# Optimization experiments

Measured on AMD Instinct MI355X. Metric: run time of the kernel, lower is better.

Reference implementation:

```python
import jax, jax.numpy as jnp
import numpy as np

DIM = 768
HEADS = 12
HIDDEN = 3072  # dim * mlp_ratio
EPS = 1e-5


def layernorm(x, g, b):
    mu = jnp.mean(x, axis=-1, keepdims=True)
    var = jnp.var(x, axis=-1, keepdims=True)
    return (x - mu) * jax.lax.rsqrt(var + EPS) * g + b


def setup_inputs() -> dict:
    key = jax.random.key(0)
    ks = jax.random.split(key, 10)
    s = 0.02
    return {
        "x": jax.random.normal(ks[0], (4, 1024, DIM), jnp.float32),
        "attention_mask": jax.random.randint(ks[1], (4, 1024), 0, 2, jnp.int32),
        "ln1_g": jnp.ones((DIM,), jnp.float32),
        "ln1_b": jnp.zeros((DIM,), jnp.float32),
        "ln2_g": jnp.ones((DIM,), jnp.float32),
        "ln2_b": jnp.zeros((DIM,), jnp.float32),
        "w_qkv": jax.random.normal(ks[2], (DIM, 3 * DIM), jnp.float32) * s,
        "b_qkv": jnp.zeros((3 * DIM,), jnp.float32),
        "w_proj": jax.random.normal(ks[3], (DIM, DIM), jnp.float32) * s,
        "b_proj": jnp.zeros((DIM,), jnp.float32),
        "w_fc1": jax.random.normal(ks[4], (DIM, HIDDEN), jnp.float32) * s,
        "b_fc1": jnp.zeros((HIDDEN,), jnp.float32),
        "w_fc2": jax.random.normal(ks[5], (HIDDEN, DIM), jnp.float32) * s,
        "b_fc2": jnp.zeros((DIM,), jnp.float32),
    }


def reference(x, attention_mask, ln1_g, ln1_b, ln2_g, ln2_b,
              w_qkv, b_qkv, w_proj, b_proj, w_fc1, b_fc1, w_fc2, b_fc2):
    B, N, C = x.shape
    hd = C // HEADS
    scale = hd ** -0.5

    # --- attention branch ---
    h = layernorm(x, ln1_g, ln1_b)
    qkv = (h @ w_qkv + b_qkv).reshape(B, N, 3, HEADS, hd)
    q, k, v = qkv[:, :, 0], qkv[:, :, 1], qkv[:, :, 2]  # [B,N,H,hd]
    attn = jnp.einsum('bnhd,bmhd->bhnm', q, k) * scale
    mask_bias = jnp.where(attention_mask == 0, -10000.0, 0.0)[:, None, None, :]
    attn = jax.nn.softmax(attn + mask_bias, axis=-1)
    o = jnp.einsum('bhnm,bmhd->bnhd', attn, v).reshape(B, N, C)
    x = x + (o @ w_proj + b_proj)

    # --- MLP branch ---
    h = layernorm(x, ln2_g, ln2_b)
    h = jax.nn.gelu(h @ w_fc1 + b_fc1, approximate=False)
    x = x + (h @ w_fc2 + b_fc2)
    return x
```

## Files before the change

### kernel.cpp

```cpp
#include <hip/hip_runtime.h>

#define DIM 768
#define NTOK 4096
#define HID 3072

typedef __attribute__((ext_vector_type(8))) short bf16x8;
typedef __attribute__((ext_vector_type(4))) float f32x4;

__device__ inline unsigned short f2bf(float f){
  unsigned u = __float_as_uint(f);
  u += 0x7fff + ((u >> 16) & 1);
  return (unsigned short)(u >> 16);
}
__device__ inline unsigned cvt_pk_bf16(float a, float b){
  unsigned r;
  asm("v_cvt_pk_bf16_f32 %0, %1, %2" : "=v"(r) : "v"(a), "v"(b));
  return r;
}
__device__ inline void gload_lds16(const void* g, void* l){
  __builtin_amdgcn_global_load_lds(
      (const __attribute__((address_space(1))) unsigned int*)g,
      (__attribute__((address_space(3))) unsigned int*)l, 16, 0, 0);
}
template<int N> __device__ inline void wait_vmcnt(){
  if constexpr (N == 0) asm volatile("s_waitcnt vmcnt(0)" ::: "memory");
  else if constexpr (N == 4) asm volatile("s_waitcnt vmcnt(4)" ::: "memory");
  else if constexpr (N == 8) asm volatile("s_waitcnt vmcnt(8)" ::: "memory");
  else static_assert(N == 0, "unsupported vmcnt");
}
__device__ inline int swz_read(int row, int hi){
  return (row * 64 + hi * 16) ^ ((row & 7) << 4);
}

__global__ __launch_bounds__(256) void ln_kernel(const float* __restrict__ x,
    const float* __restrict__ g, const float* __restrict__ b,
    unsigned short* __restrict__ out)
{
  int row = blockIdx.x * 4 + (threadIdx.x >> 6);
  int lane = threadIdx.x & 63;
  const float* xr = x + (size_t)row * DIM;
  float4 v[3];
  float s = 0.f, s2 = 0.f;
#pragma unroll
  for (int j = 0; j < 3; ++j){
    v[j] = *(const float4*)(xr + j * 256 + lane * 4);
    s  += v[j].x + v[j].y + v[j].z + v[j].w;
    s2 += v[j].x*v[j].x + v[j].y*v[j].y + v[j].z*v[j].z + v[j].w*v[j].w;
  }
#pragma unroll
  for (int m = 1; m < 64; m <<= 1){ s += __shfl_xor(s, m, 64); s2 += __shfl_xor(s2, m, 64); }
  float mu  = s * (1.f / 768.f);
  float var = s2 * (1.f / 768.f) - mu * mu;
  float inv = rsqrtf(var + 1e-5f);
#pragma unroll
  for (int j = 0; j < 3; ++j){
    int c0 = j * 256 + lane * 4;
    float vv[4] = { v[j].x, v[j].y, v[j].z, v[j].w };
    ushort4 o4;
    o4.x = f2bf((vv[0] - mu) * inv * g[c0 + 0] + b[c0 + 0]);
    o4.y = f2bf((vv[1] - mu) * inv * g[c0 + 1] + b[c0 + 1]);
    o4.z = f2bf((vv[2] - mu) * inv * g[c0 + 2] + b[c0 + 2]);
    o4.w = f2bf((vv[3] - mu) * inv * g[c0 + 3] + b[c0 + 3]);
    *(ushort4*)(out + (size_t)row * DIM + c0) = o4;
  }
}

__global__ __launch_bounds__(256) void transpose4_kernel(
    const float* __restrict__ w_qkv, const float* __restrict__ w_proj,
    const float* __restrict__ w_fc1, const float* __restrict__ w_fc2,
    unsigned short* __restrict__ tq, unsigned short* __restrict__ tp,
    unsigned short* __restrict__ t1, unsigned short* __restrict__ t2)
{
  __shared__ __align__(16) unsigned short tile[32][33];
  int id = blockIdx.x;
  const float* W; unsigned short* Wt; int K, N, tx_n;
  if (id < 1728)      { W = w_qkv;  Wt = tq; K = 768;  N = 2304; tx_n = 72; }
  else if (id < 2304) { W = w_proj; Wt = tp; K = 768;  N = 768;  tx_n = 24; id -= 1728; }
  else if (id < 4608) { W = w_fc1;  Wt = t1; K = 768;  N = 3072; tx_n = 96; id -= 2304; }
  else                { W = w_fc2;  Wt = t2; K = 3072; N = 768;  tx_n = 24; id -= 4608; }
  int n0 = (id % tx_n) * 32, k0 = (id / tx_n) * 32;
  int tx = threadIdx.x & 31, ty = threadIdx.x >> 5;
#pragma unroll
  for (int i = 0; i < 32; i += 8)
    tile[ty + i][tx] = f2bf(W[(size_t)(k0 + ty + i) * N + n0 + tx]);
  __syncthreads();
#pragma unroll
  for (int i = 0; i < 32; i += 8)
    Wt[(size_t)(n0 + ty + i) * K + k0 + tx] = tile[tx][ty + i];
}

__global__ __launch_bounds__(256) void pack_mask_kernel(const int* __restrict__ am,
    unsigned long long* __restrict__ pm)
{
  int lane = threadIdx.x & 63, w = threadIdx.x >> 6, b = blockIdx.x;
  for (int k = w; k < 16; k += 4){
    unsigned long long m = __ballot(am[b * 1024 + k * 64 + lane] != 0);
    if (lane == 0) pm[b * 16 + k] = m;
  }
}

template<int DEPTH, int EPI, typename OutT>
__global__ __launch_bounds__(256) void gemm_kernel(
    const unsigned short* __restrict__ A,
    const unsigned short* __restrict__ Bt,
    const float* __restrict__ bias,
    OutT* __restrict__ C,
    unsigned short* __restrict__ q_out,
    unsigned short* __restrict__ k_out,
    unsigned short* __restrict__ v_out,
    int M, int N, int K)
{
  constexpr int BM = 128, BN = 128, BK = 32, WM = 64, WN = 64;
  constexpr int WAVES_N = BN / WN;
  constexpr int MI = WM / 16, NI = WN / 16;
  constexpr int ACH = BM * BK / 8, BCH = BN * BK / 8;
  constexpr int NC = (ACH + BCH) / 256;
  constexpr int SMEM_B = DEPTH * (BM + BN) * BK * 2;
  __shared__ __align__(16) char smem[SMEM_B];
  auto As = (unsigned short(*)[BM * BK])smem;
  auto Bs = (unsigned short(*)[BN * BK])(smem + DEPTH * BM * BK * 2);
  const int t = threadIdx.x, lane = t & 63, wid = t >> 6;
  const int lo = lane & 15, hi = lane >> 4;
  const int wr = wid / WAVES_N, wc = wid % WAVES_N;

  const int gx = gridDim.x;
  const int nwg = gx * gridDim.y;
  const int lin = blockIdx.y * gx + blockIdx.x;
  const int swz = (lin & 7) * (nwg >> 3) + (lin >> 3);
  const int bm = (swz / gx) * BM, bn = (swz % gx) * BN;

  auto stage = [&](int buf, int k0){
#pragma unroll
    for (int u = 0; u < NC; ++u){
      int c = u * 256 + t;
      if (c < ACH){
        int rp = c >> 2, r = rp ^ ((rp >> 2) & 1), q = (c & 3) ^ (r & 3);
        gload_lds16(A + (size_t)(bm + r) * K + k0 + q * 8, &As[buf][c * 8]);
      } else {
        int c2 = c - ACH;
        int rp = c2 >> 2, r = rp ^ ((rp >> 2) & 1), q = (c2 & 3) ^ (r & 3);
        gload_lds16(Bt + (size_t)(bn + r) * K + k0 + q * 8, &Bs[buf][c2 * 8]);
      }
    }
  };

  f32x4 acc[MI][NI];
#pragma unroll
  for (int i = 0; i < MI; ++i)
#pragma unroll
    for (int j = 0; j < NI; ++j) acc[i][j] = (f32x4){0.f, 0.f, 0.f, 0.f};

  const int NIT = K / BK;
#pragma unroll
  for (int d = 0; d < DEPTH - 1; ++d) stage(d, d * BK);
  for (int it = 0; it < NIT; ++it){
    int rem = NIT - 1 - it;
    if (rem >= DEPTH - 2) wait_vmcnt<(DEPTH - 2) * NC>();
    else wait_vmcnt<0>();
    __builtin_amdgcn_sched_barrier(0);
    __builtin_amdgcn_s_barrier();
    __builtin_amdgcn_sched_barrier(0);
    if (it + DEPTH - 1 < NIT) stage((it + DEPTH - 1) % DEPTH, (it + DEPTH - 1) * BK);
    const char* as = (const char*)As[it % DEPTH];
    const char* bs = (const char*)Bs[it % DEPTH];
    bf16x8 af[MI], bfr[NI];
#pragma unroll
    for (int i = 0; i < MI; ++i){
      int row = wr * WM + i * 16 + lo;
      af[i] = *(const bf16x8*)(as + swz_read(row, hi));
    }
#pragma unroll
    for (int j = 0; j < NI; ++j){
      int row = wc * WN + j * 16 + lo;
      bfr[j] = *(const bf16x8*)(bs + swz_read(row, hi));
    }
#pragma unroll
    for (int i = 0; i < MI; ++i)
#pragma unroll
      for (int j = 0; j < NI; ++j)
        acc[i][j] = __builtin_amdgcn_mfma_f32_16x16x32_bf16(af[i], bfr[j], acc[i][j], 0, 0, 0);
  }

  __syncthreads();

  if constexpr (EPI == 0 || EPI == 1){
    constexpr int LDE = BN + 8;
    unsigned short* ET = (unsigned short*)smem;
#pragma unroll
    for (int i = 0; i < MI; ++i)
#pragma unroll
      for (int j = 0; j < NI; ++j){
        float bcol = bias[bn + wc * WN + j * 16 + lo];
#pragma unroll
        for (int r = 0; r < 4; ++r){
          float v = acc[i][j][r] + bcol;
          if constexpr (EPI == 1) v = 0.5f * v * (1.f + erff(v * 0.70710678118f));
          ET[(wr * WM + i * 16 + hi * 4 + r) * LDE + wc * WN + j * 16 + lo] = f2bf(v);
        }
      }
    __syncthreads();
#pragma unroll
    for (int p = 0; p < BM / 16; ++p){
      int row = p * 16 + (t >> 4), chunk = t & 15;
      *(bf16x8*)&((unsigned short*)C)[(size_t)(bm + row) * N + bn + chunk * 8] =
          *(const bf16x8*)&ET[row * LDE + chunk * 8];
    }
  } else {
    constexpr int LDE = BN + 8;
    unsigned short* ET = (unsigned short*)smem;
    const int part = bn / 768;
    const int cloc = bn % 768;
#pragma unroll
    for (int i = 0; i < MI; ++i)
#pragma unroll
      for (int j = 0; j < NI; ++j){
        int col_l = wc * WN + j * 16 + lo;
        float bcol = bias[bn + col_l];
#pragma unroll
        for (int r = 0; r < 4; ++r){
          int row_l = wr * WM + i * 16 + hi * 4 + r;
          unsigned short us = f2bf(acc[i][j][r] + bcol);
          if (part < 2) ET[row_l * LDE + col_l] = us;
          else          ET[col_l * LDE + row_l] = us;
        }
      }
    __syncthreads();
    const int bb = bm >> 10, n0b = bm & 1023;
    if (part < 2){
      unsigned short* dst0 = (part == 0) ? q_out : k_out;
#pragma unroll
      for (int p = 0; p < 8; ++p){
        int row = p * 16 + (t >> 4), chunk = t & 15;
        int hh = cloc / 64 + (chunk >> 3), d0 = (chunk & 7) * 8;
        unsigned short* dst = dst0 + ((size_t)(bb * 12 + hh)) * 65536 + (n0b + row) * 64 + d0;
        *(bf16x8*)dst = *(const bf16x8*)&ET[row * LDE + chunk * 8];
      }
    } else {
#pragma unroll
      for (int p = 0; p < 8; ++p){
        int colg = p * 16 + (t >> 4), chunk = t & 15;
        int hh = cloc / 64 + (colg >> 6), d = colg & 63;
        unsigned short* dst = v_out + ((size_t)(bb * 12 + hh)) * 65536 + (size_t)d * 1024 + n0b + chunk * 8;
        *(bf16x8*)dst = *(const bf16x8*)&ET[colg * LDE + chunk * 8];
      }
    }
  }
}

__global__ __launch_bounds__(512) void gemm_ks_kernel(
    const unsigned short* __restrict__ A,
    const unsigned short* __restrict__ Bt,
    const float* __restrict__ bias,
    const float* __restrict__ resid,
    float* __restrict__ C,
    int M, int N, int K)
{
  constexpr int BM = 128, BN = 96, BK = 64, DEPTH = 3;
  constexpr int MI = 4, NI = 3;
  constexpr int ACH = BM * BK / 8;
  constexpr int BCH = BN * BK / 8;
  constexpr int NC = 4;
  constexpr int TILE_A = BM * BK * 2, TILE_B = BN * BK * 2;
  constexpr int LDE = BN + 4;
  constexpr int SMEM_B = (DEPTH * (TILE_A + TILE_B) > BM * LDE * 4)
                       ?  DEPTH * (TILE_A + TILE_B) : BM * LDE * 4;
  __shared__ __align__(16) char smem[SMEM_B];
  auto As = (unsigned short(*)[BM * BK])smem;
  auto Bs = (unsigned short(*)[BN * BK])(smem + DEPTH * TILE_A);
  const int t = threadIdx.x, lane = t & 63, wid = t >> 6;
  const int lo = lane & 15, hi = lane >> 4;
  const int ks = wid & 1, wc = (wid >> 1) & 1, wr = wid >> 2;

  const int gx = gridDim.x;
  const int nwg = gx * gridDim.y;
  const int lin = blockIdx.y * gx + blockIdx.x;
  const int swz = (lin & 7) * (nwg >> 3) + (lin >> 3);
  const int bm = (swz / gx) * BM, bn = (swz % gx) * BN;

  auto stage = [&](int buf, int k0){
#pragma unroll
    for (int u = 0; u < NC; ++u){
      int c = u * 512 + t;
      if (c < ACH){
        int r = c >> 3, q = (c & 7) ^ (r & 7);
        gload_lds16(A + (size_t)(bm + r) * K + k0 + q * 8, &As[buf][c * 8]);
      } else {
        int c2 = c - ACH;
        if (c2 >= BCH) c2 -= BCH;
        int r = c2 >> 3, q = (c2 & 7) ^ (r & 7);
        gload_lds16(Bt + (size_t)(bn + r) * K + k0 + q * 8, &Bs[buf][c2 * 8]);
      }
    }
  };
  auto rd = [&](const char* base, int row, int q)->bf16x8 {
    return *(const bf16x8*)(base + row * 128 + ((q ^ (row & 7)) << 4));
  };

  f32x4 acc[MI][NI];
#pragma unroll
  for (int i = 0; i < MI; ++i)
#pragma unroll
    for (int j = 0; j < NI; ++j) acc[i][j] = (f32x4){0.f, 0.f, 0.f, 0.f};

  const int NIT = K / BK;
  stage(0, 0);
  stage(1, BK);
  const int qk = ks * 4 + hi;
  for (int it = 0; it < NIT; ++it){
    if (it < NIT - 1) wait_vmcnt<NC>();
    else wait_vmcnt<0>();
    __builtin_amdgcn_sched_barrier(0);
    __builtin_amdgcn_s_barrier();
    __builtin_amdgcn_sched_barrier(0);
    if (it + 2 < NIT) stage((it + 2) % DEPTH, (it + 2) * BK);
    const char* as = (const char*)As[it % DEPTH];
    const char* bs = (const char*)Bs[it % DEPTH];
    bf16x8 af[MI], bfr[NI];
#pragma unroll
    for (int i = 0; i < MI; ++i)  af[i]  = rd(as, wr * 64 + i * 16 + lo, qk);
#pragma unroll
    for (int j = 0; j < NI; ++j) bfr[j] = rd(bs, wc * 48 + j * 16 + lo, qk);
#pragma unroll
    for (int i = 0; i < MI; ++i)
#pragma unroll
      for (int j = 0; j < NI; ++j)
        acc[i][j] = __builtin_amdgcn_mfma_f32_16x16x32_bf16(af[i], bfr[j], acc[i][j], 0, 0, 0);
  }

  __syncthreads();
  float* ET = (float*)smem;
  if (ks == 1){
#pragma unroll
    for (int i = 0; i < MI; ++i)
#pragma unroll
      for (int j = 0; j < NI; ++j)
#pragma unroll
        for (int r = 0; r < 4; ++r)
          ET[(wr * 64 + i * 16 + hi * 4 + r) * LDE + wc * 48 + j * 16 + lo] = acc[i][j][r];
  }
  __syncthreads();
  if (ks == 0){
#pragma unroll
    for (int i = 0; i < MI; ++i)
#pragma unroll
      for (int j = 0; j < NI; ++j){
        int col_l = wc * 48 + j * 16 + lo;
        float bcol = bias[bn + col_l];
#pragma unroll
        for (int r = 0; r < 4; ++r){
          int idx = (wr * 64 + i * 16 + hi * 4 + r) * LDE + col_l;
          ET[idx] = ET[idx] + acc[i][j][r] + bcol;
        }
      }
  }
  __syncthreads();
  {
    int row = t >> 2, q = t & 3;
    const float* rrow = resid + (size_t)(bm + row) * N + bn;
    float* crow = C + (size_t)(bm + row) * N + bn;
#pragma unroll
    for (int k = 0; k < 6; ++k){
      int c4 = (q + k * 4) * 4;
      float4 v = *(const float4*)&ET[row * LDE + c4];
      float4 rs = *(const float4*)&rrow[c4];
      v.x += rs.x; v.y += rs.y; v.z += rs.z; v.w += rs.w;
      *(float4*)&crow[c4] = v;
    }
  }
}

__global__ __launch_bounds__(256) void attn_kernel(
    const unsigned short* __restrict__ Qs,
    const unsigned short* __restrict__ Ks,
    const unsigned short* __restrict__ Vts,
    const unsigned long long* __restrict__ pm,
    unsigned short* __restrict__ o)
{
  constexpr int LD = 72;
  __shared__ __align__(16) unsigned short Kl[64 * LD];
  __shared__ __align__(16) unsigned short Vt[64 * LD];
  __shared__ __align__(16) unsigned short Pl[4][16 * LD];
  const int qb = blockIdx.x, h = blockIdx.y, b = blockIdx.z;
  const int t = threadIdx.x, wid = t >> 6, lane = t & 63;
  const int lo = lane & 15, hi = lane >> 4;
  const size_t bh = (size_t)b * 12 + h;

  const unsigned short* Qg = Qs + (bh * 1024 + qb * 64 + wid * 16 + lo) * 64;
  bf16x8 qf0 = *(const bf16x8*)(Qg + hi * 8);
  bf16x8 qf1 = *(const bf16x8*)(Qg + 32 + hi * 8);

  f32x4 oacc[4];
#pragma unroll
  for (int dj = 0; dj < 4; ++dj) oacc[dj] = (f32x4){0.f, 0.f, 0.f, 0.f};
  float l_part = 0.f;

  const int srow = t >> 2, scol = (t & 3) * 16;
  const unsigned short* Kg = Ks  + bh * 65536;
  const unsigned short* Vg = Vts + bh * 65536;
  unsigned short* pw = &Pl[wid][0];

  for (int kt = 0; kt < 16; ++kt){
    __syncthreads();
    const unsigned short* kg = Kg + (kt * 64 + srow) * 64 + scol;
    *(bf16x8*)&Kl[srow * LD + scol]     = *(const bf16x8*)kg;
    *(bf16x8*)&Kl[srow * LD + scol + 8] = *(const bf16x8*)(kg + 8);
    const unsigned short* vg = Vg + srow * 1024 + kt * 64 + scol;
    *(bf16x8*)&Vt[srow * LD + scol]     = *(const bf16x8*)vg;
    *(bf16x8*)&Vt[srow * LD + scol + 8] = *(const bf16x8*)(vg + 8);
    __syncthreads();

    f32x4 s[4];
#pragma unroll
    for (int nj = 0; nj < 4; ++nj) s[nj] = (f32x4){0.f, 0.f, 0.f, 0.f};
#pragma unroll
    for (int kk = 0; kk < 2; ++kk){
      bf16x8 q = kk ? qf1 : qf0;
#pragma unroll
      for (int nj = 0; nj < 4; ++nj){
        bf16x8 kf = *(const bf16x8*)&Kl[(nj * 16 + lo) * LD + kk * 32 + hi * 8];
        s[nj] = __builtin_amdgcn_mfma_f32_16x16x32_bf16(kf, q, s[nj], 0, 0, 0);
      }
    }

    unsigned long long w = pm[b * 16 + kt] >> (hi * 4);
#pragma unroll
    for (int nj = 0; nj < 4; ++nj){
      float p[4];
#pragma unroll
      for (int r = 0; r < 4; ++r){
        float e = __expf(fmaf(s[nj][r], 0.125f, -16.0f));
        e = ((unsigned)(w >> (nj * 16 + r)) & 1u) ? e : 0.0f;
        l_part += e;
        p[r] = e;
      }
      unsigned w0 = cvt_pk_bf16(p[0], p[1]);
      unsigned w1 = cvt_pk_bf16(p[2], p[3]);
      *(uint2*)&pw[lo * LD + nj * 16 + hi * 4] = make_uint2(w0, w1);
    }
    asm volatile("" ::: "memory");
    bf16x8 pf0 = *(const bf16x8*)&pw[lo * LD + hi * 8];
    bf16x8 pf1 = *(const bf16x8*)&pw[lo * LD + 32 + hi * 8];
#pragma unroll
    for (int kk = 0; kk < 2; ++kk){
      bf16x8 pf = kk ? pf1 : pf0;
#pragma unroll
      for (int dj = 0; dj < 4; ++dj){
        bf16x8 vf = *(const bf16x8*)&Vt[(dj * 16 + lo) * LD + kk * 32 + hi * 8];
        oacc[dj] = __builtin_amdgcn_mfma_f32_16x16x32_bf16(vf, pf, oacc[dj], 0, 0, 0);
      }
    }
  }

  float l = l_part;
  l += __shfl_xor(l, 16, 64);
  l += __shfl_xor(l, 32, 64);
  float inv = 1.0f / l;
  size_t orow = (size_t)b * 1024 + qb * 64 + wid * 16 + lo;
#pragma unroll
  for (int dj = 0; dj < 4; ++dj){
    unsigned w0 = (unsigned)f2bf(oacc[dj][0] * inv) | ((unsigned)f2bf(oacc[dj][1] * inv) << 16);
    unsigned w1 = (unsigned)f2bf(oacc[dj][2] * inv) | ((unsigned)f2bf(oacc[dj][3] * inv) << 16);
    *(uint2*)&o[orow * DIM + h * 64 + dj * 16 + hi * 4] = make_uint2(w0, w1);
  }
}

extern "C" void kernel_launch(void* const* d_in, const int* in_sizes, int n_in,
                              void* d_out, int out_size, void* d_ws, size_t ws_size,
                              hipStream_t stream)
{
  const float* x      = (const float*)d_in[0];
  const int*   amask  = (const int*)  d_in[1];
  const float* ln1_g  = (const float*)d_in[2];
  const float* ln1_b  = (const float*)d_in[3];
  const float* ln2_g  = (const float*)d_in[4];
  const float* ln2_b  = (const float*)d_in[5];
  const float* w_qkv  = (const float*)d_in[6];
  const float* b_qkv  = (const float*)d_in[7];
  const float* w_proj = (const float*)d_in[8];
  const float* b_proj = (const float*)d_in[9];
  const float* w_fc1  = (const float*)d_in[10];
  const float* b_fc1  = (const float*)d_in[11];
  const float* w_fc2  = (const float*)d_in[12];
  const float* b_fc2  = (const float*)d_in[13];
  float* outp = (float*)d_out;

  char* w = (char*)d_ws;
  auto alloc = [&](size_t bytes){ char* p = w; w += (bytes + 255) & ~(size_t)255; return p; };

  char* p0 = alloc((size_t)4 * 6291456);
  unsigned short* Qs   = (unsigned short*)p0;
  unsigned short* Ks   = (unsigned short*)(p0 + 6291456);
  unsigned short* Vts  = (unsigned short*)(p0 + 2 * 6291456);
  unsigned short* o_bf = (unsigned short*)(p0 + 3 * 6291456);
  unsigned short* a1   = (unsigned short*)p0;
  unsigned short* h_bf = (unsigned short*)alloc((size_t)NTOK * DIM * 2);
  unsigned short* h2   = h_bf;
  float*          x1   = (float*)alloc((size_t)NTOK * DIM * 4);
  unsigned short* wqkvT = (unsigned short*)alloc((size_t)3 * DIM * DIM * 2);
  unsigned short* wprojT= (unsigned short*)alloc((size_t)DIM * DIM * 2);
  unsigned short* wfc1T = (unsigned short*)alloc((size_t)HID * DIM * 2);
  unsigned short* wfc2T = (unsigned short*)alloc((size_t)DIM * HID * 2);
  unsigned long long* pmask = (unsigned long long*)alloc(4 * 16 * 8);

  transpose4_kernel<<<6912, 256, 0, stream>>>(w_qkv, w_proj, w_fc1, w_fc2,
                                              wqkvT, wprojT, wfc1T, wfc2T);
  pack_mask_kernel<<<4, 256, 0, stream>>>(amask, pmask);

  ln_kernel<<<NTOK / 4, 256, 0, stream>>>(x, ln1_g, ln1_b, h_bf);
  gemm_kernel<3, 3, unsigned short><<<dim3(2304 / 128, NTOK / 128), 256, 0, stream>>>(
      h_bf, wqkvT, b_qkv, (unsigned short*)nullptr, Qs, Ks, Vts, NTOK, 2304, DIM);
  attn_kernel<<<dim3(16, 12, 4), 256, 0, stream>>>(Qs, Ks, Vts, pmask, o_bf);
  gemm_ks_kernel<<<dim3(8, NTOK / 128), 512, 0, stream>>>(
      o_bf, wprojT, b_proj, x, x1, NTOK, DIM, DIM);
  ln_kernel<<<NTOK / 4, 256, 0, stream>>>(x1, ln2_g, ln2_b, h2);
  gemm_kernel<3, 1, unsigned short><<<dim3(HID / 128, NTOK / 128), 256, 0, stream>>>(
      h2, wfc1T, b_fc1, a1, nullptr, nullptr, nullptr, NTOK, HID, DIM);
  gemm_ks_kernel<<<dim3(8, NTOK / 128), 512, 0, stream>>>(
      a1, wfc2T, b_fc2, x1, outp, NTOK, DIM, HID);
}
```

Baseline: 169.0 us.

## Unroll GEMM pipeline by depth with precomputed addresses; double-buffer attention K/V

The GEMM main loop is unrolled by three so the LDS buffer indices become compile-time constants. Global source pointers and swizzled LDS read offsets are computed once and advanced by increments, which removes per-iteration modulo and address arithmetic. The attention kernel double-buffers its K/V tiles in LDS and prefetches the next tile into registers while the current one is computed, leaving one barrier per iteration instead of two. The cost is more registers and twice the attention LDS, and the GEMM unroll assumes K/32 is a multiple of three.

```diff
diff --git a/kernel.cpp b/kernel.cpp
--- a/kernel.cpp
+++ b/kernel.cpp
@@ -99,7 +99,7 @@
   }
 }
 
-template<int DEPTH, int EPI, typename OutT>
+template<int EPI, typename OutT>
 __global__ __launch_bounds__(256) void gemm_kernel(
     const unsigned short* __restrict__ A,
     const unsigned short* __restrict__ Bt,
@@ -110,18 +110,15 @@
     unsigned short* __restrict__ v_out,
     int M, int N, int K)
 {
-  constexpr int BM = 128, BN = 128, BK = 32, WM = 64, WN = 64;
-  constexpr int WAVES_N = BN / WN;
+  constexpr int BM = 128, BN = 128, BK = 32, WM = 64, WN = 64, DEPTH = 3;
   constexpr int MI = WM / 16, NI = WN / 16;
-  constexpr int ACH = BM * BK / 8, BCH = BN * BK / 8;
-  constexpr int NC = (ACH + BCH) / 256;
   constexpr int SMEM_B = DEPTH * (BM + BN) * BK * 2;
   __shared__ __align__(16) char smem[SMEM_B];
   auto As = (unsigned short(*)[BM * BK])smem;
   auto Bs = (unsigned short(*)[BN * BK])(smem + DEPTH * BM * BK * 2);
   const int t = threadIdx.x, lane = t & 63, wid = t >> 6;
   const int lo = lane & 15, hi = lane >> 4;
-  const int wr = wid / WAVES_N, wc = wid % WAVES_N;
+  const int wr = wid >> 1, wc = wid & 1;
 
   const int gx = gridDim.x;
   const int nwg = gx * gridDim.y;
@@ -129,56 +126,62 @@
   const int swz = (lin & 7) * (nwg >> 3) + (lin >> 3);
   const int bm = (swz / gx) * BM, bn = (swz % gx) * BN;
 
-  auto stage = [&](int buf, int k0){
-#pragma unroll
-    for (int u = 0; u < NC; ++u){
-      int c = u * 256 + t;
-      if (c < ACH){
-        int rp = c >> 2, r = rp ^ ((rp >> 2) & 1), q = (c & 3) ^ (r & 3);
-        gload_lds16(A + (size_t)(bm + r) * K + k0 + q * 8, &As[buf][c * 8]);
-      } else {
-        int c2 = c - ACH;
-        int rp = c2 >> 2, r = rp ^ ((rp >> 2) & 1), q = (c2 & 3) ^ (r & 3);
-        gload_lds16(Bt + (size_t)(bn + r) * K + k0 + q * 8, &Bs[buf][c2 * 8]);
-      }
-    }
+  const unsigned short *a0, *a1, *b0, *b1;
+  {
+    int rp = t >> 2, r = rp ^ ((rp >> 2) & 1), q = (t & 3) ^ (r & 3);
+    a0 = A  + (size_t)(bm + r) * K + q * 8;
+    b0 = Bt + (size_t)(bn + r) * K + q * 8;
+    int c = 256 + t;
+    rp = c >> 2; r = rp ^ ((rp >> 2) & 1); q = (c & 3) ^ (r & 3);
+    a1 = A  + (size_t)(bm + r) * K + q * 8;
+    b1 = Bt + (size_t)(bn + r) * K + q * 8;
+  }
+  int ofsA[MI], ofsB[NI];
+#pragma unroll
+  for (int i = 0; i < MI; ++i) ofsA[i] = swz_read(wr * WM + i * 16 + lo, hi);
+#pragma unroll
+  for (int j = 0; j < NI; ++j) ofsB[j] = swz_read(wc * WN + j * 16 + lo, hi);
+
+  f32x4 acc[MI][NI];
+#pragma unroll
+  for (int i = 0; i < MI; ++i)
+#pragma unroll
+    for (int j = 0; j < NI; ++j) acc[i][j] = (f32x4){0.f, 0.f, 0.f, 0.f};
+
+  const int NIT = K / BK;
+  auto stagefull = [&](int buf) __attribute__((always_inline)) {
+    gload_lds16(a0, &As[buf][t * 8]);
+    gload_lds16(a1, &As[buf][(256 + t) * 8]);
+    gload_lds16(b0, &Bs[buf][t * 8]);
+    gload_lds16(b1, &Bs[buf][(256 + t) * 8]);
+    a0 += BK; a1 += BK; b0 += BK; b1 += BK;
   };
-
-  f32x4 acc[MI][NI];
-#pragma unroll
-  for (int i = 0; i < MI; ++i)
-#pragma unroll
-    for (int j = 0; j < NI; ++j) acc[i][j] = (f32x4){0.f, 0.f, 0.f, 0.f};
-
-  const int NIT = K / BK;
-#pragma unroll
-  for (int d = 0; d < DEPTH - 1; ++d) stage(d, d * BK);
-  for (int it = 0; it < NIT; ++it){
-    int rem = NIT - 1 - it;
-    if (rem >= DEPTH - 2) wait_vmcnt<(DEPTH - 2) * NC>();
-    else wait_vmcnt<0>();
+  auto kbody = [&](int it, int RB, int WB) __attribute__((always_inline)) {
+    if (it < NIT - 1) wait_vmcnt<4>(); else wait_vmcnt<0>();
     __builtin_amdgcn_sched_barrier(0);
     __builtin_amdgcn_s_barrier();
     __builtin_amdgcn_sched_barrier(0);
-    if (it + DEPTH - 1 < NIT) stage((it + DEPTH - 1) % DEPTH, (it + DEPTH - 1) * BK);
-    const char* as = (const char*)As[it % DEPTH];
-    const char* bs = (const char*)Bs[it % DEPTH];
+    if (it + 2 < NIT) stagefull(WB);
+    const char* as = (const char*)As[RB];
+    const char* bs = (const char*)Bs[RB];
     bf16x8 af[MI], bfr[NI];
 #pragma unroll
-    for (int i = 0; i < MI; ++i){
-      int row = wr * WM + i * 16 + lo;
-      af[i] = *(const bf16x8*)(as + swz_read(row, hi));
-    }
-#pragma unroll
-    for (int j = 0; j < NI; ++j){
-      int row = wc * WN + j * 16 + lo;
-      bfr[j] = *(const bf16x8*)(bs + swz_read(row, hi));
-    }
+    for (int i = 0; i < MI; ++i) af[i]  = *(const bf16x8*)(as + ofsA[i]);
+#pragma unroll
+    for (int j = 0; j < NI; ++j) bfr[j] = *(const bf16x8*)(bs + ofsB[j]);
 #pragma unroll
     for (int i = 0; i < MI; ++i)
 #pragma unroll
       for (int j = 0; j < NI; ++j)
         acc[i][j] = __builtin_amdgcn_mfma_f32_16x16x32_bf16(af[i], bfr[j], acc[i][j], 0, 0, 0);
+  };
+
+  stagefull(0);
+  stagefull(1);
+  for (int it = 0; it < NIT; it += 3){
+    kbody(it,     0, 2);
+    kbody(it + 1, 1, 0);
+    kbody(it + 2, 2, 1);
   }
 
   __syncthreads();
@@ -377,8 +380,8 @@
     unsigned short* __restrict__ o)
 {
   constexpr int LD = 72;
-  __shared__ __align__(16) unsigned short Kl[64 * LD];
-  __shared__ __align__(16) unsigned short Vt[64 * LD];
+  __shared__ __align__(16) unsigned short Kl[2][64 * LD];
+  __shared__ __align__(16) unsigned short Vt[2][64 * LD];
   __shared__ __align__(16) unsigned short Pl[4][16 * LD];
   const int qb = blockIdx.x, h = blockIdx.y, b = blockIdx.z;
   const int t = threadIdx.x, wid = t >> 6, lane = t & 63;
@@ -395,19 +398,29 @@
   float l_part = 0.f;
 
   const int srow = t >> 2, scol = (t & 3) * 16;
-  const unsigned short* Kg = Ks  + bh * 65536;
-  const unsigned short* Vg = Vts + bh * 65536;
+  const int sdst = srow * LD + scol;
+  const unsigned short* kg = Ks  + bh * 65536 + srow * 64 + scol;
+  const unsigned short* vg = Vts + bh * 65536 + srow * 1024 + scol;
   unsigned short* pw = &Pl[wid][0];
 
+  bf16x8 kn0 = *(const bf16x8*)(kg);
+  bf16x8 kn1 = *(const bf16x8*)(kg + 8);
+  bf16x8 vn0 = *(const bf16x8*)(vg);
+  bf16x8 vn1 = *(const bf16x8*)(vg + 8);
+  *(bf16x8*)&Kl[0][sdst]     = kn0;
+  *(bf16x8*)&Kl[0][sdst + 8] = kn1;
+  *(bf16x8*)&Vt[0][sdst]     = vn0;
+  *(bf16x8*)&Vt[0][sdst + 8] = vn1;
+  __syncthreads();
+
   for (int kt = 0; kt < 16; ++kt){
-    __syncthreads();
-    const unsigned short* kg = Kg + (kt * 64 + srow) * 64 + scol;
-    *(bf16x8*)&Kl[srow * LD + scol]     = *(const bf16x8*)kg;
-    *(bf16x8*)&Kl[srow * LD + scol + 8] = *(const bf16x8*)(kg + 8);
-    const unsigned short* vg = Vg + srow * 1024 + kt * 64 + scol;
-    *(bf16x8*)&Vt[srow * LD + scol]     = *(const bf16x8*)vg;
-    *(bf16x8*)&Vt[srow * LD + scol + 8] = *(const bf16x8*)(vg + 8);
-    __syncthreads();
+    const int cur = kt & 1;
+    if (kt + 1 < 16){
+      kn0 = *(const bf16x8*)(kg + (kt + 1) * 4096);
+      kn1 = *(const bf16x8*)(kg + (kt + 1) * 4096 + 8);
+      vn0 = *(const bf16x8*)(vg + (kt + 1) * 64);
+      vn1 = *(const bf16x8*)(vg + (kt + 1) * 64 + 8);
+    }
 
     f32x4 s[4];
 #pragma unroll
@@ -417,7 +430,7 @@
       bf16x8 q = kk ? qf1 : qf0;
 #pragma unroll
       for (int nj = 0; nj < 4; ++nj){
-        bf16x8 kf = *(const bf16x8*)&Kl[(nj * 16 + lo) * LD + kk * 32 + hi * 8];
+        bf16x8 kf = *(const bf16x8*)&Kl[cur][(nj * 16 + lo) * LD + kk * 32 + hi * 8];
         s[nj] = __builtin_amdgcn_mfma_f32_16x16x32_bf16(kf, q, s[nj], 0, 0, 0);
       }
     }
@@ -445,10 +458,18 @@
       bf16x8 pf = kk ? pf1 : pf0;
 #pragma unroll
       for (int dj = 0; dj < 4; ++dj){
-        bf16x8 vf = *(const bf16x8*)&Vt[(dj * 16 + lo) * LD + kk * 32 + hi * 8];
+        bf16x8 vf = *(const bf16x8*)&Vt[cur][(dj * 16 + lo) * LD + kk * 32 + hi * 8];
         oacc[dj] = __builtin_amdgcn_mfma_f32_16x16x32_bf16(vf, pf, oacc[dj], 0, 0, 0);
       }
     }
+
+    if (kt + 1 < 16){
+      *(bf16x8*)&Kl[cur ^ 1][sdst]     = kn0;
+      *(bf16x8*)&Kl[cur ^ 1][sdst + 8] = kn1;
+      *(bf16x8*)&Vt[cur ^ 1][sdst]     = vn0;
+      *(bf16x8*)&Vt[cur ^ 1][sdst + 8] = vn1;
+    }
+    __syncthreads();
   }
 
   float l = l_part;
@@ -507,13 +528,13 @@
   pack_mask_kernel<<<4, 256, 0, stream>>>(amask, pmask);
 
   ln_kernel<<<NTOK / 4, 256, 0, stream>>>(x, ln1_g, ln1_b, h_bf);
-  gemm_kernel<3, 3, unsigned short><<<dim3(2304 / 128, NTOK / 128), 256, 0, stream>>>(
+  gemm_kernel<3, unsigned short><<<dim3(2304 / 128, NTOK / 128), 256, 0, stream>>>(
       h_bf, wqkvT, b_qkv, (unsigned short*)nullptr, Qs, Ks, Vts, NTOK, 2304, DIM);
   attn_kernel<<<dim3(16, 12, 4), 256, 0, stream>>>(Qs, Ks, Vts, pmask, o_bf);
   gemm_ks_kernel<<<dim3(8, NTOK / 128), 512, 0, stream>>>(
       o_bf, wprojT, b_proj, x, x1, NTOK, DIM, DIM);
   ln_kernel<<<NTOK / 4, 256, 0, stream>>>(x1, ln2_g, ln2_b, h2);
-  gemm_kernel<3, 1, unsigned short><<<dim3(HID / 128, NTOK / 128), 256, 0, stream>>>(
+  gemm_kernel<1, unsigned short><<<dim3(HID / 128, NTOK / 128), 256, 0, stream>>>(
       h2, wfc1T, b_fc1, a1, nullptr, nullptr, nullptr, NTOK, HID, DIM);
   gemm_ks_kernel<<<dim3(8, NTOK / 128), 512, 0, stream>>>(
       a1, wfc2T, b_fc2, x1, outp, NTOK, DIM, HID);
```

Result: faster. 160.8 us (-4.8%).
